# Kernel tuning notes

Hardware: AMD Instinct MI355X
Metric: run time of the kernel (lower is better)

## Reference

```python
import jax, jax.numpy as jnp
import numpy as np

N_NODES = 50000
SEQ_LEN = 32
N_TOKENS = 100000
EMB_DIM = 128          # in_feats / 2
IN_FEATS = 256
N_HIDDEN = 256
N_CLASSES = 40
N_EDGES = 800000
PAD_IX = 0


def setup_inputs() -> dict:
    key = jax.random.key(0)
    k1, k2, k3, k4, k5, k6 = jax.random.split(key, 6)
    features = jax.random.randint(k1, (N_NODES, SEQ_LEN), 0, N_TOKENS, dtype=jnp.int32)
    src = jax.random.randint(k2, (N_EDGES,), 0, N_NODES, dtype=jnp.int32)
    dst = jax.random.randint(k3, (N_EDGES,), 0, N_NODES, dtype=jnp.int32)
    emb_table = jax.random.normal(k4, (N_TOKENS, EMB_DIM), dtype=jnp.float32) * 0.02
    W1 = jax.random.normal(k5, (IN_FEATS, N_HIDDEN), dtype=jnp.float32) * 0.02
    b1 = jnp.zeros((N_HIDDEN,), dtype=jnp.float32)
    W2 = jax.random.normal(k6, (N_HIDDEN, N_CLASSES), dtype=jnp.float32) * 0.02
    b2 = jnp.zeros((N_CLASSES,), dtype=jnp.float32)
    return {"features": features, "src": src, "dst": dst,
            "emb_table": emb_table, "W1": W1, "b1": b1, "W2": W2, "b2": b2}


def _apply_embs(features, emb_table):
    # padding_idx row contributes zeros (nn.Embedding padding_idx semantics)
    emb = emb_table.at[PAD_IX].set(0.0)
    h = emb[features]                                    # [N, L, D]
    seq_len = jnp.sum(features != PAD_IX, axis=1)        # [N]
    seq_len = jnp.maximum(seq_len, 1)[:, None].astype(h.dtype)
    h1 = h.sum(axis=1) / seq_len                         # masked mean
    h2 = h.max(axis=1)                                   # max pool (pads are 0)
    return jnp.concatenate((h1, h2), axis=1)             # [N, 2D]


def _graph_conv(h, src, dst, norm_s, norm_d, W, b):
    # DGL GraphConv, norm='both': out = D_in^{-1/2} A D_out^{-1/2} h W + b
    hw = h @ W                                           # transform first (smaller msgs)
    m = (hw * norm_s[:, None])[src]                      # gather messages [E, F]
    agg = jax.ops.segment_sum(m, dst, num_segments=N_NODES)
    return agg * norm_d[:, None] + b


def reference(features, src, dst, emb_table, W1, b1, W2, b2):
    ones_e = jnp.ones((src.shape[0],), dtype=jnp.float32)
    deg_out = jnp.maximum(jax.ops.segment_sum(ones_e, src, num_segments=N_NODES), 1.0)
    deg_in = jnp.maximum(jax.ops.segment_sum(ones_e, dst, num_segments=N_NODES), 1.0)
    norm_s = deg_out ** -0.5
    norm_d = deg_in ** -0.5

    h = _apply_embs(features, emb_table)                 # [N, in_feats]
    h = jax.nn.relu(_graph_conv(h, src, dst, norm_s, norm_d, W1, b1))
    # dropout is identity in eval mode
    h = _graph_conv(h, src, dst, norm_s, norm_d, W2, b2)
    return h                                             # [N, n_classes]
```

## Files before the change

kernel.cpp:

```cpp
#include <hip/hip_runtime.h>
#include <math.h>

#define N_NODES 50000
#define SEQ_LEN 32
#define EMB_DIM 128
#define IN_FEATS 256
#define N_HIDDEN 256
#define N_CLASSES 40
#define N_EDGES 800000
#define N_TOKENS 100000

#define SLOT 64
#define NBIN 196
#define BINCAP 4608
#define EPB 4000

typedef short short8 __attribute__((ext_vector_type(8)));
typedef float f32x4 __attribute__((ext_vector_type(4)));
typedef float f32x8 __attribute__((ext_vector_type(8)));

__device__ __forceinline__ unsigned short f2bf(float x) {
  unsigned int u = __float_as_uint(x);
  unsigned int r = (u + 0x7FFFu + ((u >> 16) & 1u)) >> 16;
  return (unsigned short)r;
}
__device__ __forceinline__ float bf2f(unsigned short s) {
  return __uint_as_float((unsigned int)s << 16);
}
__device__ __forceinline__ unsigned int pack2bf(float a, float b) {
  return (unsigned int)f2bf(a) | ((unsigned int)f2bf(b) << 16);
}
__device__ __forceinline__ f32x8 up8(uint4 v) {
  f32x8 f;
  f[0] = __uint_as_float(v.x << 16);
  f[1] = __uint_as_float(v.x & 0xFFFF0000u);
  f[2] = __uint_as_float(v.y << 16);
  f[3] = __uint_as_float(v.y & 0xFFFF0000u);
  f[4] = __uint_as_float(v.z << 16);
  f[5] = __uint_as_float(v.z & 0xFFFF0000u);
  f[6] = __uint_as_float(v.w << 16);
  f[7] = __uint_as_float(v.w & 0xFFFF0000u);
  return f;
}

__global__ __launch_bounds__(256) void k_pre(const int* __restrict__ src,
                                             const int* __restrict__ dst,
                                             int* __restrict__ gcntD,
                                             int* __restrict__ gcntS,
                                             unsigned int* __restrict__ dbin,
                                             unsigned char* __restrict__ sbin,
                                             const float* __restrict__ emb,
                                             unsigned short* __restrict__ emb_b,
                                             const float* __restrict__ W1,
                                             unsigned short* __restrict__ Wp1,
                                             const float* __restrict__ W2,
                                             unsigned short* __restrict__ Wp2) {
  __shared__ int cntD[NBIN], cntS[NBIN], baseD[NBIN], baseS[NBIN];
  int b = blockIdx.x, tid = threadIdx.x;
  if (b < 200) {
    if (tid < NBIN) { cntD[tid] = 0; cntS[tid] = 0; }
    __syncthreads();
    int e0 = b * EPB;
    for (int j = tid; j < EPB; j += 256) {
      int d = dst[e0 + j], s = src[e0 + j];
      atomicAdd(&cntD[d >> 8], 1);
      atomicAdd(&cntS[s >> 8], 1);
    }
    __syncthreads();
    if (tid < NBIN) {
      baseD[tid] = atomicAdd(&gcntD[tid], cntD[tid]);
      baseS[tid] = atomicAdd(&gcntS[tid], cntS[tid]);
      cntD[tid] = 0;
      cntS[tid] = 0;
    }
    __syncthreads();
    for (int j = tid; j < EPB; j += 256) {
      int d = dst[e0 + j], s = src[e0 + j];
      int bd = d >> 8, bs = s >> 8;
      int od = atomicAdd(&cntD[bd], 1);
      int pd = baseD[bd] + od;
      if (pd < BINCAP) dbin[(size_t)bd * BINCAP + pd] = ((unsigned int)s << 8) | (unsigned int)(d & 255);
      int os = atomicAdd(&cntS[bs], 1);
      int ps = baseS[bs] + os;
      if (ps < BINCAP) sbin[(size_t)bs * BINCAP + ps] = (unsigned char)(s & 255);
    }
  } else if (b < 200 + 2048) {
    const int total = N_TOKENS * EMB_DIM / 4;
    for (int i = (b - 200) * 256 + tid; i < total; i += 2048 * 256) {
      float4 v = ((const float4*)emb)[i];
      ushort4 o;
      o.x = f2bf(v.x); o.y = f2bf(v.y); o.z = f2bf(v.z); o.w = f2bf(v.w);
      ((ushort4*)emb_b)[i] = o;
    }
  } else if (b < 200 + 2048 + 32) {
    int g = (b - 2248) * 256 + tid;
    int lane = g & 63, jb = (g >> 6) & 15, kt = g >> 10;
    int col = jb * 16 + (lane & 15);
    int kbase = kt * 32 + (lane >> 4) * 8;
    unsigned short* o = Wp1 + (size_t)g * 8;
    #pragma unroll
    for (int e = 0; e < 8; ++e) o[e] = f2bf(W1[(size_t)(kbase + e) * N_HIDDEN + col]);
  } else {
    int g = (b - 2280) * 256 + tid;
    if (g < 8 * 3 * 64) {
      int lane = g & 63, jb = (g >> 6) % 3, kt = g / (3 * 64);
      int col = jb * 16 + (lane & 15);
      int kbase = kt * 32 + (lane >> 4) * 8;
      unsigned short* o = Wp2 + (size_t)g * 8;
      #pragma unroll
      for (int e = 0; e < 8; ++e)
        o[e] = (col < N_CLASSES) ? f2bf(W2[(size_t)(kbase + e) * N_CLASSES + col]) : (unsigned short)0;
    }
  }
}

__global__ __launch_bounds__(256) void k_phase2(const unsigned int* __restrict__ dbin,
                                                const int* __restrict__ gcntD,
                                                const unsigned char* __restrict__ sbin,
                                                const int* __restrict__ gcntS,
                                                int* __restrict__ cursor,
                                                int* __restrict__ csr_pad,
                                                float* __restrict__ norm_s,
                                                float* __restrict__ norm_d,
                                                const int* __restrict__ feats,
                                                const uint4* __restrict__ rows4,
                                                uint4* __restrict__ h4) {
  __shared__ int cntD[256], cntS[256];
  int tid = threadIdx.x;
  if (blockIdx.x < NBIN) {
    int b = blockIdx.x;
    cntD[tid] = 0; cntS[tid] = 0;
    __syncthreads();
    int n = min(gcntD[b], BINCAP);
    const unsigned int* bb = dbin + (size_t)b * BINCAP;
    for (int j = tid; j < n; j += 256) {
      unsigned int e = bb[j];
      int lo = e & 255;
      int slot = atomicAdd(&cntD[lo], 1);
      if (slot < SLOT) csr_pad[(size_t)(b * 256 + lo) * SLOT + slot] = (int)(e >> 8);
    }
    int ns = min(gcntS[b], BINCAP);
    const unsigned char* sb = sbin + (size_t)b * BINCAP;
    for (int j = tid; j < ns; j += 256) atomicAdd(&cntS[sb[j]], 1);
    __syncthreads();
    int node = b * 256 + tid;
    if (node < N_NODES) {
      cursor[node] = min(cntD[tid], SLOT);
      norm_d[node] = 1.0f / sqrtf((float)max(cntD[tid], 1));
      norm_s[node] = 1.0f / sqrtf((float)max(cntS[tid], 1));
    }
    return;
  }

  int w = tid >> 6, lane = tid & 63;
  int node = (blockIdx.x - NBIN) * 4 + w;
  int lq = lane & 15, qg = lane >> 4;
  int laneL = lane & 31;

  int tok0 = feats[(size_t)node * SEQ_LEN + laneL];
  unsigned long long bm = __ballot(tok0 != 0);
  int cnt = (int)__popcll(bm & 0xFFFFFFFFull);
  float inv = 1.0f / (float)max(cnt, 1);

  f32x8 s = (f32x8)(0.f);
  f32x8 mx = (f32x8)(-INFINITY);
  #pragma unroll
  for (int t = 0; t < 8; ++t) {
    int tok = __shfl(tok0, t * 4 + qg);
    uint4 v = make_uint4(0u, 0u, 0u, 0u);
    if (tok) v = rows4[(size_t)tok * 16 + lq];
    f32x8 f = up8(v);
    s += f;
    mx = __builtin_elementwise_max(mx, f);
  }
  #pragma unroll
  for (int mask = 16; mask <= 32; mask <<= 1) {
    #pragma unroll
    for (int j = 0; j < 8; ++j) {
      s[j] += __shfl_xor(s[j], mask);
      mx[j] = fmaxf(mx[j], __shfl_xor(mx[j], mask));
    }
  }
  if (qg == 0) {
    s *= inv;
    uint4* hv = h4 + (size_t)node * 32;
    hv[lq] = make_uint4(pack2bf(s[0], s[1]), pack2bf(s[2], s[3]),
                        pack2bf(s[4], s[5]), pack2bf(s[6], s[7]));
    hv[16 + lq] = make_uint4(pack2bf(mx[0], mx[1]), pack2bf(mx[2], mx[3]),
                             pack2bf(mx[4], mx[5]), pack2bf(mx[6], mx[7]));
  }
}

__global__ __launch_bounds__(256) void k_mm1(const unsigned short* __restrict__ hb,
                                             const unsigned short* __restrict__ Wp,
                                             const float* __restrict__ norm_s,
                                             unsigned short* __restrict__ out) {
  __shared__ unsigned short sA[64 * 256];
  int tid = threadIdx.x;
  int r0 = blockIdx.x * 64;
  #pragma unroll
  for (int it = 0; it < 8; ++it) {
    int idx = it * 256 + tid;
    int r = idx >> 5, kb = idx & 31;
    uint4 v = make_uint4(0, 0, 0, 0);
    int row = r0 + r;
    if (row < N_NODES) v = *(const uint4*)(hb + (size_t)row * 256 + kb * 8);
    *(uint4*)&sA[r * 256 + ((kb ^ (r & 7)) << 3)] = v;
  }
  __syncthreads();

  int w = tid >> 6, lane = tid & 63;
  const short8* W8 = (const short8*)Wp;
  f32x4 acc[4][4];
  #pragma unroll
  for (int i = 0; i < 4; ++i)
    #pragma unroll
    for (int j = 0; j < 4; ++j) acc[i][j] = (f32x4){0.f, 0.f, 0.f, 0.f};

  #pragma unroll
  for (int kt = 0; kt < 8; ++kt) {
    short8 a[4], b[4];
    int kb = kt * 4 + (lane >> 4);
    #pragma unroll
    for (int ri = 0; ri < 4; ++ri) {
      int r = ri * 16 + (lane & 15);
      a[ri] = *(const short8*)&sA[r * 256 + ((kb ^ (r & 7)) << 3)];
    }
    #pragma unroll
    for (int jb = 0; jb < 4; ++jb) b[jb] = W8[(kt * 16 + w * 4 + jb) * 64 + lane];
    #pragma unroll
    for (int ri = 0; ri < 4; ++ri)
      #pragma unroll
      for (int jb = 0; jb < 4; ++jb)
        acc[ri][jb] = __builtin_amdgcn_mfma_f32_16x16x32_bf16(a[ri], b[jb], acc[ri][jb], 0, 0, 0);
  }

  #pragma unroll
  for (int ri = 0; ri < 4; ++ri) {
    #pragma unroll
    for (int rr = 0; rr < 4; ++rr) {
      int row = r0 + ri * 16 + (lane >> 4) * 4 + rr;
      if (row < N_NODES) {
        float ns = norm_s[row];
        #pragma unroll
        for (int jb = 0; jb < 4; ++jb) {
          int col = w * 64 + jb * 16 + (lane & 15);
          out[(size_t)row * 256 + col] = f2bf(acc[ri][jb][rr] * ns);
        }
      }
    }
  }
}

__global__ __launch_bounds__(256) void k_agg1(const uint4* __restrict__ rows4,
                                              const int* __restrict__ cursor,
                                              const int* __restrict__ csr_pad,
                                              const float* __restrict__ norm_d,
                                              const float* __restrict__ b1,
                                              uint4* __restrict__ out4) {
  int tid = threadIdx.x;
  int w = tid >> 6, lane = tid & 63;
  int node = blockIdx.x * 4 + w;
  int cnt = __builtin_amdgcn_readfirstlane(cursor[node]);
  const int* csr = csr_pad + (size_t)node * SLOT;
  int half = lane >> 5, lq = lane & 31;

  f32x8 a = (f32x8)(0.f);
  int e = 0;
  for (; e + 8 <= cnt; e += 8) {
    int s0 = csr[e + 0 + half], s1 = csr[e + 2 + half];
    int s2 = csr[e + 4 + half], s3 = csr[e + 6 + half];
    uint4 v0 = rows4[(size_t)s0 * 32 + lq];
    uint4 v1 = rows4[(size_t)s1 * 32 + lq];
    uint4 v2 = rows4[(size_t)s2 * 32 + lq];
    uint4 v3 = rows4[(size_t)s3 * 32 + lq];
    a += up8(v0);
    a += up8(v1);
    a += up8(v2);
    a += up8(v3);
  }
  for (; e + 2 <= cnt; e += 2) {
    uint4 v = rows4[(size_t)csr[e + half] * 32 + lq];
    a += up8(v);
  }
  if (e < cnt) {
    uint4 v = make_uint4(0u, 0u, 0u, 0u);
    if (half == 0) v = rows4[(size_t)csr[e] * 32 + lq];
    a += up8(v);
  }
  #pragma unroll
  for (int j = 0; j < 8; ++j) a[j] += __shfl_xor(a[j], 32);

  if (half == 0) {
    float nd = norm_d[node];
    float4 bb0 = *(const float4*)&b1[8 * lq];
    float4 bb1 = *(const float4*)&b1[8 * lq + 4];
    float o0 = fmaxf(a[0] * nd + bb0.x, 0.f), o1 = fmaxf(a[1] * nd + bb0.y, 0.f);
    float o2 = fmaxf(a[2] * nd + bb0.z, 0.f), o3 = fmaxf(a[3] * nd + bb0.w, 0.f);
    float o4 = fmaxf(a[4] * nd + bb1.x, 0.f), o5 = fmaxf(a[5] * nd + bb1.y, 0.f);
    float o6 = fmaxf(a[6] * nd + bb1.z, 0.f), o7 = fmaxf(a[7] * nd + bb1.w, 0.f);
    out4[(size_t)node * 32 + lq] = make_uint4(pack2bf(o0, o1), pack2bf(o2, o3),
                                              pack2bf(o4, o5), pack2bf(o6, o7));
  }
}

__global__ __launch_bounds__(256) void k_mm2(const unsigned short* __restrict__ h2b,
                                             const unsigned short* __restrict__ Wp,
                                             const float* __restrict__ norm_s,
                                             unsigned short* __restrict__ out) {
  __shared__ unsigned short sA[64 * 256];
  int tid = threadIdx.x;
  int r0 = blockIdx.x * 64;
  #pragma unroll
  for (int it = 0; it < 8; ++it) {
    int idx = it * 256 + tid;
    int r = idx >> 5, kb = idx & 31;
    uint4 v = make_uint4(0, 0, 0, 0);
    int row = r0 + r;
    if (row < N_NODES) v = *(const uint4*)(h2b + (size_t)row * 256 + kb * 8);
    *(uint4*)&sA[r * 256 + ((kb ^ (r & 7)) << 3)] = v;
  }
  __syncthreads();

  int w = tid >> 6, lane = tid & 63;
  const short8* W8 = (const short8*)Wp;
  f32x4 acc[3];
  #pragma unroll
  for (int j = 0; j < 3; ++j) acc[j] = (f32x4){0.f, 0.f, 0.f, 0.f};

  #pragma unroll
  for (int kt = 0; kt < 8; ++kt) {
    int r = w * 16 + (lane & 15);
    int kb = kt * 4 + (lane >> 4);
    short8 a = *(const short8*)&sA[r * 256 + ((kb ^ (r & 7)) << 3)];
    #pragma unroll
    for (int jb = 0; jb < 3; ++jb) {
      short8 b = W8[(kt * 3 + jb) * 64 + lane];
      acc[jb] = __builtin_amdgcn_mfma_f32_16x16x32_bf16(a, b, acc[jb], 0, 0, 0);
    }
  }

  #pragma unroll
  for (int rr = 0; rr < 4; ++rr) {
    int row = r0 + w * 16 + (lane >> 4) * 4 + rr;
    if (row < N_NODES) {
      float ns = norm_s[row];
      #pragma unroll
      for (int jb = 0; jb < 3; ++jb) {
        int col = jb * 16 + (lane & 15);
        if (col < N_CLASSES) out[(size_t)row * N_CLASSES + col] = f2bf(acc[jb][rr] * ns);
      }
    }
  }
}

__global__ __launch_bounds__(256) void k_agg2(const uint2* __restrict__ rows2,
                                              const int* __restrict__ cursor,
                                              const int* __restrict__ csr_pad,
                                              const float* __restrict__ norm_d,
                                              const float* __restrict__ b2,
                                              float* __restrict__ out) {
  int tid = threadIdx.x;
  int w = tid >> 6, lane = tid & 63;
  int node = blockIdx.x * 4 + w;
  int slot = lane / 10, fl = lane % 10;
  int cnt = __builtin_amdgcn_readfirstlane(cursor[node]);
  const int* csr = csr_pad + (size_t)node * SLOT;

  float a0 = 0.f, a1 = 0.f, a2 = 0.f, a3 = 0.f;
  if (slot < 6) {
    for (int e = slot; e < cnt; e += 6) {
      int s = csr[e];
      uint2 v = rows2[(size_t)s * 10 + fl];
      a0 += bf2f((unsigned short)(v.x & 0xFFFF));
      a1 += bf2f((unsigned short)(v.x >> 16));
      a2 += bf2f((unsigned short)(v.y & 0xFFFF));
      a3 += bf2f((unsigned short)(v.y >> 16));
    }
  }
  float r10_0 = __shfl(a0, lane + 10), r10_1 = __shfl(a1, lane + 10), r10_2 = __shfl(a2, lane + 10), r10_3 = __shfl(a3, lane + 10);
  float r20_0 = __shfl(a0, lane + 20), r20_1 = __shfl(a1, lane + 20), r20_2 = __shfl(a2, lane + 20), r20_3 = __shfl(a3, lane + 20);
  float r30_0 = __shfl(a0, lane + 30), r30_1 = __shfl(a1, lane + 30), r30_2 = __shfl(a2, lane + 30), r30_3 = __shfl(a3, lane + 30);
  float r40_0 = __shfl(a0, lane + 40), r40_1 = __shfl(a1, lane + 40), r40_2 = __shfl(a2, lane + 40), r40_3 = __shfl(a3, lane + 40);
  float r50_0 = __shfl(a0, lane + 50), r50_1 = __shfl(a1, lane + 50), r50_2 = __shfl(a2, lane + 50), r50_3 = __shfl(a3, lane + 50);
  if (slot == 0) {
    a0 += r10_0 + r20_0 + r30_0 + r40_0 + r50_0;
    a1 += r10_1 + r20_1 + r30_1 + r40_1 + r50_1;
    a2 += r10_2 + r20_2 + r30_2 + r40_2 + r50_2;
    a3 += r10_3 + r20_3 + r30_3 + r40_3 + r50_3;
    float nd = norm_d[node];
    float4 bb = *(const float4*)&b2[4 * fl];
    float4 o = make_float4(a0 * nd + bb.x, a1 * nd + bb.y, a2 * nd + bb.z, a3 * nd + bb.w);
    *(float4*)&out[(size_t)node * N_CLASSES + 4 * fl] = o;
  }
}

extern "C" void kernel_launch(void* const* d_in, const int* in_sizes, int n_in,
                              void* d_out, int out_size, void* d_ws, size_t ws_size,
                              hipStream_t stream) {
  const int*   feats = (const int*)d_in[0];
  const int*   src   = (const int*)d_in[1];
  const int*   dst   = (const int*)d_in[2];
  const float* emb   = (const float*)d_in[3];
  const float* W1    = (const float*)d_in[4];
  const float* b1    = (const float*)d_in[5];
  const float* W2    = (const float*)d_in[6];
  const float* b2    = (const float*)d_in[7];
  float* out = (float*)d_out;

  char* base = (char*)d_ws;
  size_t off = 0;
  auto alloc = [&](size_t bytes) -> char* {
    char* p = base + off;
    off += (bytes + 255) & ~(size_t)255;
    return p;
  };
  unsigned short* hb      = (unsigned short*)alloc((size_t)N_NODES * IN_FEATS * 2);
  unsigned short* msgb    = (unsigned short*)alloc((size_t)N_NODES * N_HIDDEN * 2);
  unsigned short* hw2b    = (unsigned short*)alloc((size_t)N_NODES * N_CLASSES * 2);
  unsigned short* emb_b   = (unsigned short*)alloc((size_t)N_TOKENS * EMB_DIM * 2);
  unsigned short* Wp1     = (unsigned short*)alloc((size_t)8 * 16 * 64 * 8 * 2);
  unsigned short* Wp2     = (unsigned short*)alloc((size_t)8 * 3 * 64 * 8 * 2);
  int*   gcnt    = (int*)alloc((size_t)512 * 4);
  int*   gcntD   = gcnt;
  int*   gcntS   = gcnt + 256;
  int*   cursor  = (int*)alloc((size_t)N_NODES * 4);
  float* norm_s  = (float*)alloc((size_t)N_NODES * 4);
  float* norm_d  = (float*)alloc((size_t)N_NODES * 4);
  unsigned int*  dbin = (unsigned int*)alloc((size_t)NBIN * BINCAP * 4);
  unsigned char* sbin = (unsigned char*)alloc((size_t)NBIN * BINCAP);
  int*   csr_pad = (int*)alloc((size_t)N_NODES * SLOT * 4);

  hipMemsetAsync(gcnt, 0, 512 * 4, stream);

  k_pre<<<200 + 2048 + 32 + 6, 256, 0, stream>>>(src, dst, gcntD, gcntS, dbin, sbin,
                                                 emb, emb_b, W1, Wp1, W2, Wp2);
  k_phase2<<<NBIN + N_NODES / 4, 256, 0, stream>>>(dbin, gcntD, sbin, gcntS, cursor, csr_pad,
                                                   norm_s, norm_d,
                                                   feats, (const uint4*)emb_b, (uint4*)hb);

  int gemm_blocks = (N_NODES + 63) / 64;
  k_mm1<<<gemm_blocks, 256, 0, stream>>>(hb, Wp1, norm_s, msgb);
  k_agg1<<<N_NODES / 4, 256, 0, stream>>>((const uint4*)msgb, cursor, csr_pad, norm_d, b1, (uint4*)hb);
  k_mm2<<<gemm_blocks, 256, 0, stream>>>(hb, Wp2, norm_s, hw2b);
  k_agg2<<<N_NODES / 4, 256, 0, stream>>>((const uint2*)hw2b, cursor, csr_pad, norm_d, b2, out);
}
```

Baseline: 203.1 us.

## Fuse all stages into one persistent cooperative kernel with grid syncs

Merges the six separate kernels (binning, CSR build plus embedding pooling, two GEMMs, two aggregations) into one persistent cooperative kernel. Work items are spread over a grid sized from occupancy, and stages are separated by grid.sync. This removes the launch gaps and tail drain between kernel boundaries. In exchange it caps the grid at resident blocks, uses 32KB of shared memory in every stage, and adds grid-wide barrier costs, which could lower occupancy for the gather-heavy stages.

Result: slower. 596.0 us (+193.5%).

```diff
diff --git a/kernel.cpp b/kernel.cpp
--- a/kernel.cpp
+++ b/kernel.cpp
@@ -1,5 +1,8 @@
 #include <hip/hip_runtime.h>
+#include <hip/hip_cooperative_groups.h>
 #include <math.h>
+
+namespace cg = cooperative_groups;
 
 #define N_NODES 50000
 #define SEQ_LEN 32
@@ -43,355 +46,353 @@
   return f;
 }
 
-__global__ __launch_bounds__(256) void k_pre(const int* __restrict__ src,
-                                             const int* __restrict__ dst,
-                                             int* __restrict__ gcntD,
-                                             int* __restrict__ gcntS,
-                                             unsigned int* __restrict__ dbin,
-                                             unsigned char* __restrict__ sbin,
-                                             const float* __restrict__ emb,
-                                             unsigned short* __restrict__ emb_b,
-                                             const float* __restrict__ W1,
-                                             unsigned short* __restrict__ Wp1,
-                                             const float* __restrict__ W2,
-                                             unsigned short* __restrict__ Wp2) {
-  __shared__ int cntD[NBIN], cntS[NBIN], baseD[NBIN], baseS[NBIN];
-  int b = blockIdx.x, tid = threadIdx.x;
-  if (b < 200) {
-    if (tid < NBIN) { cntD[tid] = 0; cntS[tid] = 0; }
-    __syncthreads();
-    int e0 = b * EPB;
-    for (int j = tid; j < EPB; j += 256) {
-      int d = dst[e0 + j], s = src[e0 + j];
-      atomicAdd(&cntD[d >> 8], 1);
-      atomicAdd(&cntS[s >> 8], 1);
-    }
-    __syncthreads();
-    if (tid < NBIN) {
-      baseD[tid] = atomicAdd(&gcntD[tid], cntD[tid]);
-      baseS[tid] = atomicAdd(&gcntS[tid], cntS[tid]);
-      cntD[tid] = 0;
-      cntS[tid] = 0;
-    }
-    __syncthreads();
-    for (int j = tid; j < EPB; j += 256) {
-      int d = dst[e0 + j], s = src[e0 + j];
-      int bd = d >> 8, bs = s >> 8;
-      int od = atomicAdd(&cntD[bd], 1);
-      int pd = baseD[bd] + od;
-      if (pd < BINCAP) dbin[(size_t)bd * BINCAP + pd] = ((unsigned int)s << 8) | (unsigned int)(d & 255);
-      int os = atomicAdd(&cntS[bs], 1);
-      int ps = baseS[bs] + os;
-      if (ps < BINCAP) sbin[(size_t)bs * BINCAP + ps] = (unsigned char)(s & 255);
-    }
-  } else if (b < 200 + 2048) {
-    const int total = N_TOKENS * EMB_DIM / 4;
-    for (int i = (b - 200) * 256 + tid; i < total; i += 2048 * 256) {
-      float4 v = ((const float4*)emb)[i];
-      ushort4 o;
-      o.x = f2bf(v.x); o.y = f2bf(v.y); o.z = f2bf(v.z); o.w = f2bf(v.w);
-      ((ushort4*)emb_b)[i] = o;
-    }
-  } else if (b < 200 + 2048 + 32) {
-    int g = (b - 2248) * 256 + tid;
-    int lane = g & 63, jb = (g >> 6) & 15, kt = g >> 10;
-    int col = jb * 16 + (lane & 15);
-    int kbase = kt * 32 + (lane >> 4) * 8;
-    unsigned short* o = Wp1 + (size_t)g * 8;
-    #pragma unroll
-    for (int e = 0; e < 8; ++e) o[e] = f2bf(W1[(size_t)(kbase + e) * N_HIDDEN + col]);
-  } else {
-    int g = (b - 2280) * 256 + tid;
-    if (g < 8 * 3 * 64) {
-      int lane = g & 63, jb = (g >> 6) % 3, kt = g / (3 * 64);
-      int col = jb * 16 + (lane & 15);
-      int kbase = kt * 32 + (lane >> 4) * 8;
-      unsigned short* o = Wp2 + (size_t)g * 8;
-      #pragma unroll
-      for (int e = 0; e < 8; ++e)
-        o[e] = (col < N_CLASSES) ? f2bf(W2[(size_t)(kbase + e) * N_CLASSES + col]) : (unsigned short)0;
-    }
-  }
-}
-
-__global__ __launch_bounds__(256) void k_phase2(const unsigned int* __restrict__ dbin,
-                                                const int* __restrict__ gcntD,
-                                                const unsigned char* __restrict__ sbin,
-                                                const int* __restrict__ gcntS,
-                                                int* __restrict__ cursor,
-                                                int* __restrict__ csr_pad,
-                                                float* __restrict__ norm_s,
-                                                float* __restrict__ norm_d,
-                                                const int* __restrict__ feats,
-                                                const uint4* __restrict__ rows4,
-                                                uint4* __restrict__ h4) {
-  __shared__ int cntD[256], cntS[256];
-  int tid = threadIdx.x;
-  if (blockIdx.x < NBIN) {
-    int b = blockIdx.x;
-    cntD[tid] = 0; cntS[tid] = 0;
-    __syncthreads();
-    int n = min(gcntD[b], BINCAP);
-    const unsigned int* bb = dbin + (size_t)b * BINCAP;
-    for (int j = tid; j < n; j += 256) {
-      unsigned int e = bb[j];
-      int lo = e & 255;
-      int slot = atomicAdd(&cntD[lo], 1);
-      if (slot < SLOT) csr_pad[(size_t)(b * 256 + lo) * SLOT + slot] = (int)(e >> 8);
-    }
-    int ns = min(gcntS[b], BINCAP);
-    const unsigned char* sb = sbin + (size_t)b * BINCAP;
-    for (int j = tid; j < ns; j += 256) atomicAdd(&cntS[sb[j]], 1);
-    __syncthreads();
-    int node = b * 256 + tid;
-    if (node < N_NODES) {
-      cursor[node] = min(cntD[tid], SLOT);
-      norm_d[node] = 1.0f / sqrtf((float)max(cntD[tid], 1));
-      norm_s[node] = 1.0f / sqrtf((float)max(cntS[tid], 1));
-    }
-    return;
-  }
-
-  int w = tid >> 6, lane = tid & 63;
-  int node = (blockIdx.x - NBIN) * 4 + w;
-  int lq = lane & 15, qg = lane >> 4;
-  int laneL = lane & 31;
-
-  int tok0 = feats[(size_t)node * SEQ_LEN + laneL];
-  unsigned long long bm = __ballot(tok0 != 0);
-  int cnt = (int)__popcll(bm & 0xFFFFFFFFull);
-  float inv = 1.0f / (float)max(cnt, 1);
-
-  f32x8 s = (f32x8)(0.f);
-  f32x8 mx = (f32x8)(-INFINITY);
-  #pragma unroll
-  for (int t = 0; t < 8; ++t) {
-    int tok = __shfl(tok0, t * 4 + qg);
-    uint4 v = make_uint4(0u, 0u, 0u, 0u);
-    if (tok) v = rows4[(size_t)tok * 16 + lq];
-    f32x8 f = up8(v);
-    s += f;
-    mx = __builtin_elementwise_max(mx, f);
-  }
-  #pragma unroll
-  for (int mask = 16; mask <= 32; mask <<= 1) {
-    #pragma unroll
-    for (int j = 0; j < 8; ++j) {
-      s[j] += __shfl_xor(s[j], mask);
-      mx[j] = fmaxf(mx[j], __shfl_xor(mx[j], mask));
-    }
-  }
-  if (qg == 0) {
-    s *= inv;
-    uint4* hv = h4 + (size_t)node * 32;
-    hv[lq] = make_uint4(pack2bf(s[0], s[1]), pack2bf(s[2], s[3]),
-                        pack2bf(s[4], s[5]), pack2bf(s[6], s[7]));
-    hv[16 + lq] = make_uint4(pack2bf(mx[0], mx[1]), pack2bf(mx[2], mx[3]),
-                             pack2bf(mx[4], mx[5]), pack2bf(mx[6], mx[7]));
-  }
-}
-
-__global__ __launch_bounds__(256) void k_mm1(const unsigned short* __restrict__ hb,
-                                             const unsigned short* __restrict__ Wp,
-                                             const float* __restrict__ norm_s,
-                                             unsigned short* __restrict__ out) {
+__global__ __launch_bounds__(256) void k_all(
+    const int* __restrict__ src, const int* __restrict__ dst,
+    int* __restrict__ gcntD, int* __restrict__ gcntS,
+    unsigned int* __restrict__ dbin, unsigned char* __restrict__ sbin,
+    const float* __restrict__ emb, unsigned short* __restrict__ emb_b,
+    const float* __restrict__ W1, unsigned short* __restrict__ Wp1,
+    const float* __restrict__ W2, unsigned short* __restrict__ Wp2,
+    const int* __restrict__ feats,
+    int* __restrict__ cursor, int* __restrict__ csr_pad,
+    float* __restrict__ norm_s, float* __restrict__ norm_d,
+    unsigned short* __restrict__ hb, unsigned short* __restrict__ msgb,
+    unsigned short* __restrict__ hw2b,
+    const float* __restrict__ b1v, const float* __restrict__ b2v,
+    float* __restrict__ outp) {
+  cg::grid_group grid = cg::this_grid();
   __shared__ unsigned short sA[64 * 256];
   int tid = threadIdx.x;
-  int r0 = blockIdx.x * 64;
-  #pragma unroll
-  for (int it = 0; it < 8; ++it) {
-    int idx = it * 256 + tid;
-    int r = idx >> 5, kb = idx & 31;
-    uint4 v = make_uint4(0, 0, 0, 0);
-    int row = r0 + r;
-    if (row < N_NODES) v = *(const uint4*)(hb + (size_t)row * 256 + kb * 8);
-    *(uint4*)&sA[r * 256 + ((kb ^ (r & 7)) << 3)] = v;
-  }
-  __syncthreads();
-
   int w = tid >> 6, lane = tid & 63;
-  const short8* W8 = (const short8*)Wp;
-  f32x4 acc[4][4];
-  #pragma unroll
-  for (int i = 0; i < 4; ++i)
-    #pragma unroll
-    for (int j = 0; j < 4; ++j) acc[i][j] = (f32x4){0.f, 0.f, 0.f, 0.f};
-
-  #pragma unroll
-  for (int kt = 0; kt < 8; ++kt) {
-    short8 a[4], b[4];
-    int kb = kt * 4 + (lane >> 4);
-    #pragma unroll
-    for (int ri = 0; ri < 4; ++ri) {
-      int r = ri * 16 + (lane & 15);
-      a[ri] = *(const short8*)&sA[r * 256 + ((kb ^ (r & 7)) << 3)];
-    }
-    #pragma unroll
-    for (int jb = 0; jb < 4; ++jb) b[jb] = W8[(kt * 16 + w * 4 + jb) * 64 + lane];
-    #pragma unroll
-    for (int ri = 0; ri < 4; ++ri)
-      #pragma unroll
-      for (int jb = 0; jb < 4; ++jb)
-        acc[ri][jb] = __builtin_amdgcn_mfma_f32_16x16x32_bf16(a[ri], b[jb], acc[ri][jb], 0, 0, 0);
-  }
-
-  #pragma unroll
-  for (int ri = 0; ri < 4; ++ri) {
-    #pragma unroll
-    for (int rr = 0; rr < 4; ++rr) {
-      int row = r0 + ri * 16 + (lane >> 4) * 4 + rr;
-      if (row < N_NODES) {
-        float ns = norm_s[row];
-        #pragma unroll
-        for (int jb = 0; jb < 4; ++jb) {
-          int col = w * 64 + jb * 16 + (lane & 15);
-          out[(size_t)row * 256 + col] = f2bf(acc[ri][jb][rr] * ns);
-        }
-      }
-    }
-  }
-}
-
-__global__ __launch_bounds__(256) void k_agg1(const uint4* __restrict__ rows4,
-                                              const int* __restrict__ cursor,
-                                              const int* __restrict__ csr_pad,
-                                              const float* __restrict__ norm_d,
-                                              const float* __restrict__ b1,
-                                              uint4* __restrict__ out4) {
-  int tid = threadIdx.x;
-  int w = tid >> 6, lane = tid & 63;
-  int node = blockIdx.x * 4 + w;
-  int cnt = __builtin_amdgcn_readfirstlane(cursor[node]);
-  const int* csr = csr_pad + (size_t)node * SLOT;
-  int half = lane >> 5, lq = lane & 31;
-
-  f32x8 a = (f32x8)(0.f);
-  int e = 0;
-  for (; e + 8 <= cnt; e += 8) {
-    int s0 = csr[e + 0 + half], s1 = csr[e + 2 + half];
-    int s2 = csr[e + 4 + half], s3 = csr[e + 6 + half];
-    uint4 v0 = rows4[(size_t)s0 * 32 + lq];
-    uint4 v1 = rows4[(size_t)s1 * 32 + lq];
-    uint4 v2 = rows4[(size_t)s2 * 32 + lq];
-    uint4 v3 = rows4[(size_t)s3 * 32 + lq];
-    a += up8(v0);
-    a += up8(v1);
-    a += up8(v2);
-    a += up8(v3);
-  }
-  for (; e + 2 <= cnt; e += 2) {
-    uint4 v = rows4[(size_t)csr[e + half] * 32 + lq];
-    a += up8(v);
-  }
-  if (e < cnt) {
-    uint4 v = make_uint4(0u, 0u, 0u, 0u);
-    if (half == 0) v = rows4[(size_t)csr[e] * 32 + lq];
-    a += up8(v);
-  }
-  #pragma unroll
-  for (int j = 0; j < 8; ++j) a[j] += __shfl_xor(a[j], 32);
-
-  if (half == 0) {
-    float nd = norm_d[node];
-    float4 bb0 = *(const float4*)&b1[8 * lq];
-    float4 bb1 = *(const float4*)&b1[8 * lq + 4];
-    float o0 = fmaxf(a[0] * nd + bb0.x, 0.f), o1 = fmaxf(a[1] * nd + bb0.y, 0.f);
-    float o2 = fmaxf(a[2] * nd + bb0.z, 0.f), o3 = fmaxf(a[3] * nd + bb0.w, 0.f);
-    float o4 = fmaxf(a[4] * nd + bb1.x, 0.f), o5 = fmaxf(a[5] * nd + bb1.y, 0.f);
-    float o6 = fmaxf(a[6] * nd + bb1.z, 0.f), o7 = fmaxf(a[7] * nd + bb1.w, 0.f);
-    out4[(size_t)node * 32 + lq] = make_uint4(pack2bf(o0, o1), pack2bf(o2, o3),
-                                              pack2bf(o4, o5), pack2bf(o6, o7));
-  }
-}
-
-__global__ __launch_bounds__(256) void k_mm2(const unsigned short* __restrict__ h2b,
-                                             const unsigned short* __restrict__ Wp,
-                                             const float* __restrict__ norm_s,
-                                             unsigned short* __restrict__ out) {
-  __shared__ unsigned short sA[64 * 256];
-  int tid = threadIdx.x;
-  int r0 = blockIdx.x * 64;
-  #pragma unroll
-  for (int it = 0; it < 8; ++it) {
-    int idx = it * 256 + tid;
-    int r = idx >> 5, kb = idx & 31;
-    uint4 v = make_uint4(0, 0, 0, 0);
-    int row = r0 + r;
-    if (row < N_NODES) v = *(const uint4*)(h2b + (size_t)row * 256 + kb * 8);
-    *(uint4*)&sA[r * 256 + ((kb ^ (r & 7)) << 3)] = v;
-  }
-  __syncthreads();
-
-  int w = tid >> 6, lane = tid & 63;
-  const short8* W8 = (const short8*)Wp;
-  f32x4 acc[3];
-  #pragma unroll
-  for (int j = 0; j < 3; ++j) acc[j] = (f32x4){0.f, 0.f, 0.f, 0.f};
-
-  #pragma unroll
-  for (int kt = 0; kt < 8; ++kt) {
-    int r = w * 16 + (lane & 15);
-    int kb = kt * 4 + (lane >> 4);
-    short8 a = *(const short8*)&sA[r * 256 + ((kb ^ (r & 7)) << 3)];
-    #pragma unroll
-    for (int jb = 0; jb < 3; ++jb) {
-      short8 b = W8[(kt * 3 + jb) * 64 + lane];
-      acc[jb] = __builtin_amdgcn_mfma_f32_16x16x32_bf16(a, b, acc[jb], 0, 0, 0);
-    }
-  }
-
-  #pragma unroll
-  for (int rr = 0; rr < 4; ++rr) {
-    int row = r0 + w * 16 + (lane >> 4) * 4 + rr;
-    if (row < N_NODES) {
-      float ns = norm_s[row];
-      #pragma unroll
-      for (int jb = 0; jb < 3; ++jb) {
-        int col = jb * 16 + (lane & 15);
-        if (col < N_CLASSES) out[(size_t)row * N_CLASSES + col] = f2bf(acc[jb][rr] * ns);
-      }
-    }
-  }
-}
-
-__global__ __launch_bounds__(256) void k_agg2(const uint2* __restrict__ rows2,
-                                              const int* __restrict__ cursor,
-                                              const int* __restrict__ csr_pad,
-                                              const float* __restrict__ norm_d,
-                                              const float* __restrict__ b2,
-                                              float* __restrict__ out) {
-  int tid = threadIdx.x;
-  int w = tid >> 6, lane = tid & 63;
-  int node = blockIdx.x * 4 + w;
-  int slot = lane / 10, fl = lane % 10;
-  int cnt = __builtin_amdgcn_readfirstlane(cursor[node]);
-  const int* csr = csr_pad + (size_t)node * SLOT;
-
-  float a0 = 0.f, a1 = 0.f, a2 = 0.f, a3 = 0.f;
-  if (slot < 6) {
-    for (int e = slot; e < cnt; e += 6) {
-      int s = csr[e];
-      uint2 v = rows2[(size_t)s * 10 + fl];
-      a0 += bf2f((unsigned short)(v.x & 0xFFFF));
-      a1 += bf2f((unsigned short)(v.x >> 16));
-      a2 += bf2f((unsigned short)(v.y & 0xFFFF));
-      a3 += bf2f((unsigned short)(v.y >> 16));
-    }
-  }
-  float r10_0 = __shfl(a0, lane + 10), r10_1 = __shfl(a1, lane + 10), r10_2 = __shfl(a2, lane + 10), r10_3 = __shfl(a3, lane + 10);
-  float r20_0 = __shfl(a0, lane + 20), r20_1 = __shfl(a1, lane + 20), r20_2 = __shfl(a2, lane + 20), r20_3 = __shfl(a3, lane + 20);
-  float r30_0 = __shfl(a0, lane + 30), r30_1 = __shfl(a1, lane + 30), r30_2 = __shfl(a2, lane + 30), r30_3 = __shfl(a3, lane + 30);
-  float r40_0 = __shfl(a0, lane + 40), r40_1 = __shfl(a1, lane + 40), r40_2 = __shfl(a2, lane + 40), r40_3 = __shfl(a3, lane + 40);
-  float r50_0 = __shfl(a0, lane + 50), r50_1 = __shfl(a1, lane + 50), r50_2 = __shfl(a2, lane + 50), r50_3 = __shfl(a3, lane + 50);
-  if (slot == 0) {
-    a0 += r10_0 + r20_0 + r30_0 + r40_0 + r50_0;
-    a1 += r10_1 + r20_1 + r30_1 + r40_1 + r50_1;
-    a2 += r10_2 + r20_2 + r30_2 + r40_2 + r50_2;
-    a3 += r10_3 + r20_3 + r30_3 + r40_3 + r50_3;
-    float nd = norm_d[node];
-    float4 bb = *(const float4*)&b2[4 * fl];
-    float4 o = make_float4(a0 * nd + bb.x, a1 * nd + bb.y, a2 * nd + bb.z, a3 * nd + bb.w);
-    *(float4*)&out[(size_t)node * N_CLASSES + 4 * fl] = o;
+
+  {
+    int* cntD = (int*)sA;
+    int* cntS = cntD + 256;
+    int* baseD = cntS + 256;
+    int* baseS = baseD + 256;
+    for (int b = blockIdx.x; b < 200 + 2048 + 32 + 6; b += gridDim.x) {
+      if (b < 200) {
+        if (tid < NBIN) { cntD[tid] = 0; cntS[tid] = 0; }
+        __syncthreads();
+        int e0 = b * EPB;
+        for (int j = tid; j < EPB; j += 256) {
+          int d = dst[e0 + j], s = src[e0 + j];
+          atomicAdd(&cntD[d >> 8], 1);
+          atomicAdd(&cntS[s >> 8], 1);
+        }
+        __syncthreads();
+        if (tid < NBIN) {
+          baseD[tid] = atomicAdd(&gcntD[tid], cntD[tid]);
+          baseS[tid] = atomicAdd(&gcntS[tid], cntS[tid]);
+          cntD[tid] = 0;
+          cntS[tid] = 0;
+        }
+        __syncthreads();
+        for (int j = tid; j < EPB; j += 256) {
+          int d = dst[e0 + j], s = src[e0 + j];
+          int bd = d >> 8, bs = s >> 8;
+          int od = atomicAdd(&cntD[bd], 1);
+          int pd = baseD[bd] + od;
+          if (pd < BINCAP) dbin[(size_t)bd * BINCAP + pd] = ((unsigned int)s << 8) | (unsigned int)(d & 255);
+          int os = atomicAdd(&cntS[bs], 1);
+          int ps = baseS[bs] + os;
+          if (ps < BINCAP) sbin[(size_t)bs * BINCAP + ps] = (unsigned char)(s & 255);
+        }
+        __syncthreads();
+      } else if (b < 200 + 2048) {
+        const int total = N_TOKENS * EMB_DIM / 4;
+        for (int i = (b - 200) * 256 + tid; i < total; i += 2048 * 256) {
+          float4 v = ((const float4*)emb)[i];
+          ushort4 o;
+          o.x = f2bf(v.x); o.y = f2bf(v.y); o.z = f2bf(v.z); o.w = f2bf(v.w);
+          ((ushort4*)emb_b)[i] = o;
+        }
+      } else if (b < 200 + 2048 + 32) {
+        int g = (b - 2248) * 256 + tid;
+        int ln = g & 63, jb = (g >> 6) & 15, kt = g >> 10;
+        int col = jb * 16 + (ln & 15);
+        int kbase = kt * 32 + (ln >> 4) * 8;
+        unsigned short* o = Wp1 + (size_t)g * 8;
+        #pragma unroll
+        for (int e = 0; e < 8; ++e) o[e] = f2bf(W1[(size_t)(kbase + e) * N_HIDDEN + col]);
+      } else {
+        int g = (b - 2280) * 256 + tid;
+        if (g < 8 * 3 * 64) {
+          int ln = g & 63, jb = (g >> 6) % 3, kt = g / (3 * 64);
+          int col = jb * 16 + (ln & 15);
+          int kbase = kt * 32 + (ln >> 4) * 8;
+          unsigned short* o = Wp2 + (size_t)g * 8;
+          #pragma unroll
+          for (int e = 0; e < 8; ++e)
+            o[e] = (col < N_CLASSES) ? f2bf(W2[(size_t)(kbase + e) * N_CLASSES + col]) : (unsigned short)0;
+        }
+      }
+    }
+  }
+  grid.sync();
+
+  {
+    int* cntD = (int*)sA;
+    int* cntS = cntD + 256;
+    for (int b = blockIdx.x; b < NBIN + N_NODES / 4; b += gridDim.x) {
+      if (b < NBIN) {
+        cntD[tid] = 0; cntS[tid] = 0;
+        __syncthreads();
+        int n = min(gcntD[b], BINCAP);
+        const unsigned int* bb = dbin + (size_t)b * BINCAP;
+        for (int j = tid; j < n; j += 256) {
+          unsigned int e = bb[j];
+          int lo = e & 255;
+          int slot = atomicAdd(&cntD[lo], 1);
+          if (slot < SLOT) csr_pad[(size_t)(b * 256 + lo) * SLOT + slot] = (int)(e >> 8);
+        }
+        int ns = min(gcntS[b], BINCAP);
+        const unsigned char* sb = sbin + (size_t)b * BINCAP;
+        for (int j = tid; j < ns; j += 256) atomicAdd(&cntS[sb[j]], 1);
+        __syncthreads();
+        int node = b * 256 + tid;
+        if (node < N_NODES) {
+          cursor[node] = min(cntD[tid], SLOT);
+          norm_d[node] = 1.0f / sqrtf((float)max(cntD[tid], 1));
+          norm_s[node] = 1.0f / sqrtf((float)max(cntS[tid], 1));
+        }
+        __syncthreads();
+      } else {
+        const uint4* rows4 = (const uint4*)emb_b;
+        uint4* h4 = (uint4*)hb;
+        int node = (b - NBIN) * 4 + w;
+        int lq = lane & 15, qg = lane >> 4;
+        int laneL = lane & 31;
+
+        int tok0 = feats[(size_t)node * SEQ_LEN + laneL];
+        unsigned long long bm = __ballot(tok0 != 0);
+        int cnt = (int)__popcll(bm & 0xFFFFFFFFull);
+        float inv = 1.0f / (float)max(cnt, 1);
+
+        f32x8 s = (f32x8)(0.f);
+        f32x8 mx = (f32x8)(-INFINITY);
+        #pragma unroll
+        for (int t = 0; t < 8; ++t) {
+          int tok = __shfl(tok0, t * 4 + qg);
+          uint4 v = make_uint4(0u, 0u, 0u, 0u);
+          if (tok) v = rows4[(size_t)tok * 16 + lq];
+          f32x8 f = up8(v);
+          s += f;
+          mx = __builtin_elementwise_max(mx, f);
+        }
+        #pragma unroll
+        for (int mask = 16; mask <= 32; mask <<= 1) {
+          #pragma unroll
+          for (int j = 0; j < 8; ++j) {
+            s[j] += __shfl_xor(s[j], mask);
+            mx[j] = fmaxf(mx[j], __shfl_xor(mx[j], mask));
+          }
+        }
+        if (qg == 0) {
+          s *= inv;
+          uint4* hv = h4 + (size_t)node * 32;
+          hv[lq] = make_uint4(pack2bf(s[0], s[1]), pack2bf(s[2], s[3]),
+                              pack2bf(s[4], s[5]), pack2bf(s[6], s[7]));
+          hv[16 + lq] = make_uint4(pack2bf(mx[0], mx[1]), pack2bf(mx[2], mx[3]),
+                                   pack2bf(mx[4], mx[5]), pack2bf(mx[6], mx[7]));
+        }
+      }
+    }
+  }
+  grid.sync();
+
+  {
+    const short8* W8 = (const short8*)Wp1;
+    for (int u = blockIdx.x; u < (N_NODES + 63) / 64; u += gridDim.x) {
+      int r0 = u * 64;
+      #pragma unroll
+      for (int it = 0; it < 8; ++it) {
+        int idx = it * 256 + tid;
+        int r = idx >> 5, kb = idx & 31;
+        uint4 v = make_uint4(0, 0, 0, 0);
+        int row = r0 + r;
+        if (row < N_NODES) v = *(const uint4*)(hb + (size_t)row * 256 + kb * 8);
+        *(uint4*)&sA[r * 256 + ((kb ^ (r & 7)) << 3)] = v;
+      }
+      __syncthreads();
+
+      f32x4 acc[4][4];
+      #pragma unroll
+      for (int i = 0; i < 4; ++i)
+        #pragma unroll
+        for (int j = 0; j < 4; ++j) acc[i][j] = (f32x4){0.f, 0.f, 0.f, 0.f};
+
+      #pragma unroll
+      for (int kt = 0; kt < 8; ++kt) {
+        short8 a[4], bv[4];
+        int kb = kt * 4 + (lane >> 4);
+        #pragma unroll
+        for (int ri = 0; ri < 4; ++ri) {
+          int r = ri * 16 + (lane & 15);
+          a[ri] = *(const short8*)&sA[r * 256 + ((kb ^ (r & 7)) << 3)];
+        }
+        #pragma unroll
+        for (int jb = 0; jb < 4; ++jb) bv[jb] = W8[(kt * 16 + w * 4 + jb) * 64 + lane];
+        #pragma unroll
+        for (int ri = 0; ri < 4; ++ri)
+          #pragma unroll
+          for (int jb = 0; jb < 4; ++jb)
+            acc[ri][jb] = __builtin_amdgcn_mfma_f32_16x16x32_bf16(a[ri], bv[jb], acc[ri][jb], 0, 0, 0);
+      }
+
+      #pragma unroll
+      for (int ri = 0; ri < 4; ++ri) {
+        #pragma unroll
+        for (int rr = 0; rr < 4; ++rr) {
+          int row = r0 + ri * 16 + (lane >> 4) * 4 + rr;
+          if (row < N_NODES) {
+            float ns = norm_s[row];
+            #pragma unroll
+            for (int jb = 0; jb < 4; ++jb) {
+              int col = w * 64 + jb * 16 + (lane & 15);
+              msgb[(size_t)row * 256 + col] = f2bf(acc[ri][jb][rr] * ns);
+            }
+          }
+        }
+      }
+      __syncthreads();
+    }
+  }
+  grid.sync();
+
+  {
+    const uint4* rows4 = (const uint4*)msgb;
+    uint4* out4 = (uint4*)hb;
+    int half = lane >> 5, lq = lane & 31;
+    for (int u = blockIdx.x; u < N_NODES / 4; u += gridDim.x) {
+      int node = u * 4 + w;
+      int cnt = __builtin_amdgcn_readfirstlane(cursor[node]);
+      const int* csr = csr_pad + (size_t)node * SLOT;
+
+      f32x8 a = (f32x8)(0.f);
+      int e = 0;
+      for (; e + 8 <= cnt; e += 8) {
+        int s0 = csr[e + 0 + half], s1 = csr[e + 2 + half];
+        int s2 = csr[e + 4 + half], s3 = csr[e + 6 + half];
+        uint4 v0 = rows4[(size_t)s0 * 32 + lq];
+        uint4 v1 = rows4[(size_t)s1 * 32 + lq];
+        uint4 v2 = rows4[(size_t)s2 * 32 + lq];
+        uint4 v3 = rows4[(size_t)s3 * 32 + lq];
+        a += up8(v0);
+        a += up8(v1);
+        a += up8(v2);
+        a += up8(v3);
+      }
+      for (; e + 2 <= cnt; e += 2) {
+        uint4 v = rows4[(size_t)csr[e + half] * 32 + lq];
+        a += up8(v);
+      }
+      if (e < cnt) {
+        uint4 v = make_uint4(0u, 0u, 0u, 0u);
+        if (half == 0) v = rows4[(size_t)csr[e] * 32 + lq];
+        a += up8(v);
+      }
+      #pragma unroll
+      for (int j = 0; j < 8; ++j) a[j] += __shfl_xor(a[j], 32);
+
+      if (half == 0) {
+        float nd = norm_d[node];
+        float4 bb0 = *(const float4*)&b1v[8 * lq];
+        float4 bb1 = *(const float4*)&b1v[8 * lq + 4];
+        float o0 = fmaxf(a[0] * nd + bb0.x, 0.f), o1 = fmaxf(a[1] * nd + bb0.y, 0.f);
+        float o2 = fmaxf(a[2] * nd + bb0.z, 0.f), o3 = fmaxf(a[3] * nd + bb0.w, 0.f);
+        float o4 = fmaxf(a[4] * nd + bb1.x, 0.f), o5 = fmaxf(a[5] * nd + bb1.y, 0.f);
+        float o6 = fmaxf(a[6] * nd + bb1.z, 0.f), o7 = fmaxf(a[7] * nd + bb1.w, 0.f);
+        out4[(size_t)node * 32 + lq] = make_uint4(pack2bf(o0, o1), pack2bf(o2, o3),
+                                                  pack2bf(o4, o5), pack2bf(o6, o7));
+      }
+    }
+  }
+  grid.sync();
+
+  {
+    const short8* W8 = (const short8*)Wp2;
+    for (int u = blockIdx.x; u < (N_NODES + 63) / 64; u += gridDim.x) {
+      int r0 = u * 64;
+      #pragma unroll
+      for (int it = 0; it < 8; ++it) {
+        int idx = it * 256 + tid;
+        int r = idx >> 5, kb = idx & 31;
+        uint4 v = make_uint4(0, 0, 0, 0);
+        int row = r0 + r;
+        if (row < N_NODES) v = *(const uint4*)(hb + (size_t)row * 256 + kb * 8);
+        *(uint4*)&sA[r * 256 + ((kb ^ (r & 7)) << 3)] = v;
+      }
+      __syncthreads();
+
+      f32x4 acc[3];
+      #pragma unroll
+      for (int j = 0; j < 3; ++j) acc[j] = (f32x4){0.f, 0.f, 0.f, 0.f};
+
+      #pragma unroll
+      for (int kt = 0; kt < 8; ++kt) {
+        int r = w * 16 + (lane & 15);
+        int kb = kt * 4 + (lane >> 4);
+        short8 a = *(const short8*)&sA[r * 256 + ((kb ^ (r & 7)) << 3)];
+        #pragma unroll
+        for (int jb = 0; jb < 3; ++jb) {
+          short8 bv = W8[(kt * 3 + jb) * 64 + lane];
+          acc[jb] = __builtin_amdgcn_mfma_f32_16x16x32_bf16(a, bv, acc[jb], 0, 0, 0);
+        }
+      }
+
+      #pragma unroll
+      for (int rr = 0; rr < 4; ++rr) {
+        int row = r0 + w * 16 + (lane >> 4) * 4 + rr;
+        if (row < N_NODES) {
+          float ns = norm_s[row];
+          #pragma unroll
+          for (int jb = 0; jb < 3; ++jb) {
+            int col = jb * 16 + (lane & 15);
+            if (col < N_CLASSES) hw2b[(size_t)row * N_CLASSES + col] = f2bf(acc[jb][rr] * ns);
+          }
+        }
+      }
+      __syncthreads();
+    }
+  }
+  grid.sync();
+
+  {
+    const uint2* rows2 = (const uint2*)hw2b;
+    int slot = lane / 10, fl = lane % 10;
+    for (int u = blockIdx.x; u < N_NODES / 4; u += gridDim.x) {
+      int node = u * 4 + w;
+      int cnt = __builtin_amdgcn_readfirstlane(cursor[node]);
+      const int* csr = csr_pad + (size_t)node * SLOT;
+
+      float a0 = 0.f, a1 = 0.f, a2 = 0.f, a3 = 0.f;
+      if (slot < 6) {
+        for (int e = slot; e < cnt; e += 6) {
+          int s = csr[e];
+          uint2 v = rows2[(size_t)s * 10 + fl];
+          a0 += bf2f((unsigned short)(v.x & 0xFFFF));
+          a1 += bf2f((unsigned short)(v.x >> 16));
+          a2 += bf2f((unsigned short)(v.y & 0xFFFF));
+          a3 += bf2f((unsigned short)(v.y >> 16));
+        }
+      }
+      float r10_0 = __shfl(a0, lane + 10), r10_1 = __shfl(a1, lane + 10), r10_2 = __shfl(a2, lane + 10), r10_3 = __shfl(a3, lane + 10);
+      float r20_0 = __shfl(a0, lane + 20), r20_1 = __shfl(a1, lane + 20), r20_2 = __shfl(a2, lane + 20), r20_3 = __shfl(a3, lane + 20);
+      float r30_0 = __shfl(a0, lane + 30), r30_1 = __shfl(a1, lane + 30), r30_2 = __shfl(a2, lane + 30), r30_3 = __shfl(a3, lane + 30);
+      float r40_0 = __shfl(a0, lane + 40), r40_1 = __shfl(a1, lane + 40), r40_2 = __shfl(a2, lane + 40), r40_3 = __shfl(a3, lane + 40);
+      float r50_0 = __shfl(a0, lane + 50), r50_1 = __shfl(a1, lane + 50), r50_2 = __shfl(a2, lane + 50), r50_3 = __shfl(a3, lane + 50);
+      if (slot == 0) {
+        a0 += r10_0 + r20_0 + r30_0 + r40_0 + r50_0;
+        a1 += r10_1 + r20_1 + r30_1 + r40_1 + r50_1;
+        a2 += r10_2 + r20_2 + r30_2 + r40_2 + r50_2;
+        a3 += r10_3 + r20_3 + r30_3 + r40_3 + r50_3;
+        float nd = norm_d[node];
+        float4 bb = *(const float4*)&b2v[4 * fl];
+        float4 o = make_float4(a0 * nd + bb.x, a1 * nd + bb.y, a2 * nd + bb.z, a3 * nd + bb.w);
+        *(float4*)&outp[(size_t)node * N_CLASSES + 4 * fl] = o;
+      }
+    }
   }
 }
 
@@ -433,15 +434,19 @@
 
   hipMemsetAsync(gcnt, 0, 512 * 4, stream);
 
-  k_pre<<<200 + 2048 + 32 + 6, 256, 0, stream>>>(src, dst, gcntD, gcntS, dbin, sbin,
-                                                 emb, emb_b, W1, Wp1, W2, Wp2);
-  k_phase2<<<NBIN + N_NODES / 4, 256, 0, stream>>>(dbin, gcntD, sbin, gcntS, cursor, csr_pad,
-                                                   norm_s, norm_d,
-                                                   feats, (const uint4*)emb_b, (uint4*)hb);
-
-  int gemm_blocks = (N_NODES + 63) / 64;
-  k_mm1<<<gemm_blocks, 256, 0, stream>>>(hb, Wp1, norm_s, msgb);
-  k_agg1<<<N_NODES / 4, 256, 0, stream>>>((const uint4*)msgb, cursor, csr_pad, norm_d, b1, (uint4*)hb);
-  k_mm2<<<gemm_blocks, 256, 0, stream>>>(hb, Wp2, norm_s, hw2b);
-  k_agg2<<<N_NODES / 4, 256, 0, stream>>>((const uint2*)hw2b, cursor, csr_pad, norm_d, b2, out);
-}
+  int maxb = 0;
+  hipOccupancyMaxActiveBlocksPerMultiprocessor(&maxb, (const void*)k_all, 256, 0);
+  if (maxb < 1) maxb = 1;
+  int grid = maxb * 256;
+  if (grid > 2048) grid = 2048;
+
+  void* args[] = {
+    (void*)&src, (void*)&dst, (void*)&gcntD, (void*)&gcntS,
+    (void*)&dbin, (void*)&sbin, (void*)&emb, (void*)&emb_b,
+    (void*)&W1, (void*)&Wp1, (void*)&W2, (void*)&Wp2,
+    (void*)&feats, (void*)&cursor, (void*)&csr_pad,
+    (void*)&norm_s, (void*)&norm_d, (void*)&hb, (void*)&msgb,
+    (void*)&hw2b, (void*)&b1, (void*)&b2, (void*)&out
+  };
+  hipLaunchCooperativeKernel((const void*)k_all, dim3(grid), dim3(256), args, 0, stream);
+}
```
